# Kernel tuning notes

Hardware: AMD Instinct MI355X
Metric: run time of the kernel (lower is better)

The kernel has to match this reference:

```python
import jax, jax.numpy as jnp
import numpy as np
from jax import lax

B, T, E, H, FD, V = 64, 30, 300, 512, 512, 10000


def setup_inputs() -> dict:
    key = jax.random.key(0)
    ks = iter(jax.random.split(key, 64))

    def nrm(shape, s=0.02):
        return jax.random.normal(next(ks), shape, jnp.float32) * s

    inp = {}
    inp["captions"] = jax.random.randint(next(ks), (B, T), 0, V)
    inp["features"] = jax.random.normal(next(ks), (B, E), jnp.float32)
    inp["h0"] = jax.random.uniform(next(ks), (B, H), jnp.float32)
    inp["c0"] = jax.random.uniform(next(ks), (B, H), jnp.float32)
    inp["B_emb"] = nrm((V, E), 1.0)  # nn.Embedding default N(0,1)
    for g in "ifoc":
        inp[f"V_{g}_W"] = nrm((E, FD)); inp[f"V_{g}_b"] = jnp.zeros((FD,), jnp.float32)
        inp[f"S_{g}_W"] = nrm((FD, FD)); inp[f"S_{g}_b"] = jnp.zeros((FD,), jnp.float32)
        inp[f"U_{g}_W"] = nrm((FD, H)); inp[f"U_{g}_b"] = jnp.zeros((H,), jnp.float32)
        inp[f"W_{g}_W"] = nrm((H, H)); inp[f"W_{g}_b"] = jnp.zeros((H,), jnp.float32)
    inp["C_W"] = nrm((H, V)); inp["C_b"] = jnp.zeros((V,), jnp.float32)
    return inp


def _factored_lstm(captions, features, h0, c0, B_emb,
                   V_i_W, V_i_b, S_i_W, S_i_b, U_i_W, U_i_b, W_i_W, W_i_b,
                   V_f_W, V_f_b, S_f_W, S_f_b, U_f_W, U_f_b, W_f_W, W_f_b,
                   V_o_W, V_o_b, S_o_W, S_o_b, U_o_W, U_o_b, W_o_W, W_o_b,
                   V_c_W, V_c_b, S_c_W, S_c_b, U_c_W, U_c_b, W_c_W, W_c_b,
                   C_W, C_b):
    # mode == 'factual': prepend image features as first timestep
    emb = B_emb[captions]                                       # [B,T,E]
    x = jnp.concatenate([features[:, None, :], emb], axis=1)[:, :-1]  # [B,T,E]

    # input-dependent gate pre-activations: U_g(S_fg(V_g(x))) are h-independent,
    # so precompute them for all timesteps (same math, batched GEMMs).
    def pre(Vw, Vb, Sw, Sb, Uw, Ub):
        f = (x @ Vw + Vb) @ Sw + Sb                             # [B,T,FD]
        return (f @ Uw + Ub).transpose(1, 0, 2)                 # [T,B,H]

    ui = pre(V_i_W, V_i_b, S_i_W, S_i_b, U_i_W, U_i_b)
    uf = pre(V_f_W, V_f_b, S_f_W, S_f_b, U_f_W, U_f_b)
    uo = pre(V_o_W, V_o_b, S_o_W, S_o_b, U_o_W, U_o_b)
    uc = pre(V_c_W, V_c_b, S_c_W, S_c_b, U_c_W, U_c_b)

    def step(carry, u):
        h, c = carry
        gi, gf, go, gc = u
        i_t = jax.nn.sigmoid(gi + h @ W_i_W + W_i_b)
        f_t = jax.nn.sigmoid(gf + h @ W_f_W + W_f_b)
        o_t = jax.nn.sigmoid(go + h @ W_o_W + W_o_b)
        c_tilda = jnp.tanh(gc + h @ W_c_W + W_c_b)
        c_t = f_t * c + i_t * c_tilda
        h_t = o_t * c_t                                         # note: no tanh, as in source
        out = h_t @ C_W + C_b                                   # [B,V]
        return (h_t, c_t), out

    (_, _), outs = lax.scan(step, (h0, c0), (ui, uf, uo, uc))   # outs [T,B,V]
    return outs.transpose(1, 0, 2)                              # [B,T,V]


def reference(captions, features, h0, c0, B_emb,
              V_i_W, V_i_b, S_i_W, S_i_b, U_i_W, U_i_b, W_i_W, W_i_b,
              V_f_W, V_f_b, S_f_W, S_f_b, U_f_W, U_f_b, W_f_W, W_f_b,
              V_o_W, V_o_b, S_o_W, S_o_b, U_o_W, U_o_b, W_o_W, W_o_b,
              V_c_W, V_c_b, S_c_W, S_c_b, U_c_W, U_c_b, W_c_W, W_c_b,
              C_W, C_b):
    return _factored_lstm(captions, features, h0, c0, B_emb,
                          V_i_W, V_i_b, S_i_W, S_i_b, U_i_W, U_i_b, W_i_W, W_i_b,
                          V_f_W, V_f_b, S_f_W, S_f_b, U_f_W, U_f_b, W_f_W, W_f_b,
                          V_o_W, V_o_b, S_o_W, S_o_b, U_o_W, U_o_b, W_o_W, W_o_b,
                          V_c_W, V_c_b, S_c_W, S_c_b, U_c_W, U_c_b, W_c_W, W_c_b,
                          C_W, C_b)
```

## Files before the change

### kernel.cpp

```cpp
#include <hip/hip_runtime.h>
#include <hip/hip_bf16.h>

#define B_  64
#define T_  30
#define E_  300
#define H_  512
#define FD_ 512
#define V_  10000
#define NR_ 32
#define NPW_ 224
#define NTN_ 79
#define NTG_ 8
#define AGGF_ 1056

typedef __attribute__((ext_vector_type(8))) unsigned short ushort8_t;
typedef __attribute__((ext_vector_type(4))) unsigned short ushort4_t;
typedef __attribute__((ext_vector_type(8))) __bf16 bf16x8;
typedef __attribute__((ext_vector_type(4))) float f32x4;

__device__ __forceinline__ float b2f(unsigned short u) {
    union { unsigned int i; float f; } v;
    v.i = ((unsigned int)u) << 16;
    return v.f;
}
__device__ __forceinline__ unsigned short f2b(float f) {
    unsigned int x = __builtin_bit_cast(unsigned int, f);
    unsigned int r = x + 0x7FFFu + ((x >> 16) & 1u);
    return (unsigned short)(r >> 16);
}
__device__ __forceinline__ f32x4 mfma16(bf16x8 a, bf16x8 b, f32x4 c) {
    return __builtin_amdgcn_mfma_f32_16x16x32_bf16(a, b, c, 0, 0, 0);
}

struct PrepA {
    const float* tsrc[17];
    unsigned short* tdst[17];
    const int* captions;
    const float* features;
    const float* Bemb;
    unsigned short* X;
    const float* h0;
    unsigned short* cH0;
    int* bar;
};

__global__ __launch_bounds__(256) void prep_k(PrepA p) {
    const int blk = blockIdx.x, tid = threadIdx.x;
    __shared__ unsigned short tile[32][33];
    if (blk < 8720) {
        int z, bx, by, R, C, Rpad, ld;
        if (blk < 3072) { z = blk >> 8; int wq = blk & 255; bx = wq & 15; by = wq >> 4; R = 512; C = 512; Rpad = 512; ld = 512; }
        else if (blk < 3712) { int b2 = blk - 3072; z = 12 + b2 / 160; int wq = b2 % 160; bx = wq & 15; by = wq >> 4; R = 300; C = 512; Rpad = 320; ld = 320; }
        else { int b2 = blk - 3712; z = 16; bx = b2 % 313; by = b2 / 313; R = 512; C = 10000; Rpad = 512; ld = 512; }
        const float* __restrict__ src = p.tsrc[z];
        unsigned short* __restrict__ dst = p.tdst[z];
        const int tc = tid & 31, tr = tid >> 5;
        const int c0 = bx * 32, r0 = by * 32;
#pragma unroll
        for (int i = 0; i < 4; ++i) {
            int r = r0 + tr + i * 8, c = c0 + tc;
            unsigned short v = 0;
            if (r < R && c < C) v = f2b(src[(size_t)r * C + c]);
            tile[tr + i * 8][tc] = v;
        }
        __syncthreads();
#pragma unroll
        for (int i = 0; i < 4; ++i) {
            int c = c0 + tr + i * 8;
            int r = r0 + tc;
            if (c < C && r < Rpad) dst[(size_t)c * ld + r] = tile[tc][tr + i * 8];
        }
    } else if (blk < 11000) {
        int idx = (blk - 8720) * 256 + tid;
        if (idx < B_ * T_ * 304) {
            int r = idx / 304, e = idx - r * 304;
            int t = r >> 6, b = r & 63;
            float v = 0.f;
            if (e < E_) {
                if (t == 0) v = p.features[b * E_ + e];
                else {
                    int tok = p.captions[b * T_ + (t - 1)];
                    v = p.Bemb[(size_t)tok * E_ + e];
                }
            }
            p.X[(size_t)r * 304 + e] = f2b(v);
        }
    } else {
        int i = (blk - 11000) * 256 + tid;
        if (i < 2048) p.bar[i] = 0;
        if (i < B_ * H_) p.cH0[i] = f2b(p.h0[i]);
    }
}

struct ChainA {
    const unsigned short* X;
    const unsigned short* Vt[4];
    const float* Vb[4];
    const unsigned short* St[4];
    const float* Sb[4];
    const unsigned short* Ut[4];
    const float* Ub[4];
    unsigned short* U[4];
};

__global__ __launch_bounds__(256) void chain_k(ChainA ca) {
    const int rb = blockIdx.x >> 2, g = blockIdx.x & 3;
    __shared__ char pool[66560];
    unsigned short* XT = (unsigned short*)pool;
    unsigned short* R0 = (unsigned short*)pool;
    unsigned short* R1 = (unsigned short*)(pool + 33280);
    const int tid = threadIdx.x;
    const int wv = tid >> 6, lane = tid & 63;
    const int quad = lane >> 4, l16 = lane & 15;

    {
        const unsigned short* src = ca.X + (size_t)rb * 32 * 304;
#pragma unroll
        for (int it = 0; it < 5; ++it) {
            int id = it * 256 + tid;
            int row = id / 40, c8 = (id % 40) * 8;
            ushort8_t v = {0, 0, 0, 0, 0, 0, 0, 0};
            if (c8 < 304) v = *(const ushort8_t*)(src + row * 304 + c8);
            *(ushort8_t*)&XT[row * 328 + c8] = v;
        }
    }
    __syncthreads();
#pragma unroll
    for (int half = 0; half < 2; ++half) {
        const int cb = wv * 128 + half * 64;
        f32x4 acc[2][4] = {};
        for (int kc = 0; kc < 10; ++kc) {
            bf16x8 af[2];
#pragma unroll
            for (int mt = 0; mt < 2; ++mt)
                af[mt] = *(const bf16x8*)&XT[(mt * 16 + l16) * 328 + kc * 32 + quad * 8];
#pragma unroll
            for (int nt = 0; nt < 4; ++nt) {
                bf16x8 bf = *(const bf16x8*)(ca.Vt[g] + (size_t)(cb + nt * 16 + l16) * 320 + kc * 32 + quad * 8);
#pragma unroll
                for (int mt = 0; mt < 2; ++mt) acc[mt][nt] = mfma16(af[mt], bf, acc[mt][nt]);
            }
        }
#pragma unroll
        for (int mt = 0; mt < 2; ++mt)
#pragma unroll
            for (int nt = 0; nt < 4; ++nt) {
                int col = cb + nt * 16 + l16;
                float bv = ca.Vb[g][col];
#pragma unroll
                for (int r = 0; r < 4; ++r)
                    R1[(mt * 16 + quad * 4 + r) * 520 + col] = f2b(acc[mt][nt][r] + bv);
            }
    }
    __syncthreads();
#pragma unroll
    for (int half = 0; half < 2; ++half) {
        const int cb = wv * 128 + half * 64;
        f32x4 acc[2][4] = {};
        for (int kc = 0; kc < 16; ++kc) {
            bf16x8 af[2];
#pragma unroll
            for (int mt = 0; mt < 2; ++mt)
                af[mt] = *(const bf16x8*)&R1[(mt * 16 + l16) * 520 + kc * 32 + quad * 8];
#pragma unroll
            for (int nt = 0; nt < 4; ++nt) {
                bf16x8 bf = *(const bf16x8*)(ca.St[g] + (size_t)(cb + nt * 16 + l16) * 512 + kc * 32 + quad * 8);
#pragma unroll
                for (int mt = 0; mt < 2; ++mt) acc[mt][nt] = mfma16(af[mt], bf, acc[mt][nt]);
            }
        }
        __syncthreads();
#pragma unroll
        for (int mt = 0; mt < 2; ++mt)
#pragma unroll
            for (int nt = 0; nt < 4; ++nt) {
                int col = cb + nt * 16 + l16;
                float bv = ca.Sb[g][col];
#pragma unroll
                for (int r = 0; r < 4; ++r)
                    R0[(mt * 16 + quad * 4 + r) * 520 + col] = f2b(acc[mt][nt][r] + bv);
            }
    }
    __syncthreads();
#pragma unroll
    for (int half = 0; half < 2; ++half) {
        const int cb = wv * 128 + half * 64;
        f32x4 acc[2][4] = {};
        for (int kc = 0; kc < 16; ++kc) {
            bf16x8 af[2];
#pragma unroll
            for (int mt = 0; mt < 2; ++mt)
                af[mt] = *(const bf16x8*)&R0[(mt * 16 + l16) * 520 + kc * 32 + quad * 8];
#pragma unroll
            for (int nt = 0; nt < 4; ++nt) {
                bf16x8 bf = *(const bf16x8*)(ca.Ut[g] + (size_t)(cb + nt * 16 + l16) * 512 + kc * 32 + quad * 8);
#pragma unroll
                for (int mt = 0; mt < 2; ++mt) acc[mt][nt] = mfma16(af[mt], bf, acc[mt][nt]);
            }
        }
#pragma unroll
        for (int mt = 0; mt < 2; ++mt)
#pragma unroll
            for (int nt = 0; nt < 4; ++nt) {
                int col = cb + nt * 16 + l16;
                float bv = ca.Ub[g][col];
#pragma unroll
                for (int r = 0; r < 4; ++r)
                    ca.U[g][(size_t)(rb * 32 + mt * 16 + quad * 4 + r) * 512 + col] =
                        f2b(acc[mt][nt][r] + bv);
            }
    }
}

struct MegaA {
    const unsigned short* h0c;
    const unsigned short* Wt[4];
    const float* Wb[4];
    const unsigned short* U[4];
    const float* c0;
    unsigned short* Hall;
    int* bar;
    const unsigned short* Ct;
    const float* Cb;
    float* out;
};

__global__ __launch_bounds__(256, 1) void mega_k(MegaA a) {
    __shared__ char pool[83712];
    const int tid = threadIdx.x;
    const int lane = tid & 63;
    const int quad = lane >> 4, l16 = lane & 15;

    if (blockIdx.x < NR_) {
        unsigned short* hs = (unsigned short*)pool;
        float* xch = (float*)(pool + 66560);
        const int j = blockIdx.x;
        const int g = tid >> 6;
        bf16x8 afrag[16];
        {
            const unsigned short* wt = a.Wt[g] + (size_t)(j * 16 + l16) * H_ + quad * 8;
#pragma unroll
            for (int kc = 0; kc < 16; ++kc) afrag[kc] = *(const bf16x8*)(wt + kc * 32);
        }
        const int eb = tid >> 2;
        const int ehc = (tid & 3) * 4;
        const int hcg = j * 16 + ehc;
        f32x4 wb[4];
#pragma unroll
        for (int q = 0; q < 4; ++q) wb[q] = *(const f32x4*)(a.Wb[q] + hcg);
        f32x4 c = *(const f32x4*)(a.c0 + (size_t)eb * H_ + hcg);

        for (int t = 0; t < T_; ++t) {
            ushort4_t u[4];
#pragma unroll
            for (int q = 0; q < 4; ++q)
                u[q] = *(const ushort4_t*)(a.U[q] + ((size_t)t * B_ + eb) * H_ + hcg);
            const unsigned short* hp = t ? (a.Hall + (size_t)(t - 1) * B_ * H_) : a.h0c;
#pragma unroll
            for (int it = 0; it < 16; ++it) {
                int id = it * 256 + tid;
                int row = id >> 6, c8 = (id & 63) * 8;
                ushort8_t v = *(const ushort8_t*)(hp + row * H_ + c8);
                *(ushort8_t*)&hs[row * 520 + c8] = v;
            }
            __syncthreads();
            f32x4 acc[4] = {{0.f,0.f,0.f,0.f},{0.f,0.f,0.f,0.f},{0.f,0.f,0.f,0.f},{0.f,0.f,0.f,0.f}};
#pragma unroll
            for (int kc = 0; kc < 16; ++kc) {
#pragma unroll
                for (int nt = 0; nt < 4; ++nt) {
                    bf16x8 bfr = *(const bf16x8*)&hs[(nt * 16 + l16) * 520 + kc * 32 + quad * 8];
                    acc[nt] = mfma16(afrag[kc], bfr, acc[nt]);
                }
            }
#pragma unroll
            for (int nt = 0; nt < 4; ++nt)
#pragma unroll
                for (int r = 0; r < 4; ++r)
                    xch[g * 1040 + (quad * 4 + r) * 65 + nt * 16 + l16] = acc[nt][r];
            __syncthreads();
            ushort4_t hnew;
#pragma unroll
            for (int r = 0; r < 4; ++r) {
                float pi = xch[0 * 1040 + (ehc + r) * 65 + eb] + b2f(u[0][r]) + wb[0][r];
                float pf = xch[1 * 1040 + (ehc + r) * 65 + eb] + b2f(u[1][r]) + wb[1][r];
                float po = xch[2 * 1040 + (ehc + r) * 65 + eb] + b2f(u[2][r]) + wb[2][r];
                float pc = xch[3 * 1040 + (ehc + r) * 65 + eb] + b2f(u[3][r]) + wb[3][r];
                float it = 1.f / (1.f + __expf(-pi));
                float ft = 1.f / (1.f + __expf(-pf));
                float ot = 1.f / (1.f + __expf(-po));
                float ct = tanhf(pc);
                float cn = ft * c[r] + it * ct;
                c[r] = cn;
                hnew[r] = f2b(ot * cn);
            }
            {
                union { ushort4_t s4; unsigned long long q; } hu;
                hu.s4 = hnew;
                __hip_atomic_store((unsigned long long*)(a.Hall + ((size_t)t * B_ + eb) * H_ + hcg),
                                   hu.q, __ATOMIC_RELAXED, __HIP_MEMORY_SCOPE_AGENT);
            }
            asm volatile("s_waitcnt vmcnt(0)" ::: "memory");
            __syncthreads();
            if (tid == 0)
                __hip_atomic_store(&a.bar[j], t + 1, __ATOMIC_RELAXED, __HIP_MEMORY_SCOPE_AGENT);
            if (t + 1 < T_ || j == 0) {
                if (g == 0) {
                    bool done;
                    do {
                        int v = __hip_atomic_load(&a.bar[lane & 31], __ATOMIC_RELAXED, __HIP_MEMORY_SCOPE_AGENT);
                        done = __all(v >= t + 1);
                        if (!done) __builtin_amdgcn_s_sleep(1);
                    } while (!done);
                    if (j == 0 && lane == 0)
                        __hip_atomic_store(&a.bar[AGGF_], t + 1, __ATOMIC_RELAXED, __HIP_MEMORY_SCOPE_AGENT);
                }
                if (t + 1 < T_) __syncthreads();
            }
        }
    } else {
        unsigned short* As = (unsigned short*)pool;
        unsigned short* Bs = (unsigned short*)(pool + 36864);
        const int wv = tid >> 6;
        const int mw = (wv & 1) * 32, nw = (wv >> 1) * 64;
        const int NJ = NTG_ * NTN_;
        int hiF = 0;
        for (int q = (int)blockIdx.x - NR_; q < NJ; q += NPW_) {
            const int tg = q / NTN_, n0 = (q % NTN_) * 128;
            const int tb = tg * 4;
            const int need = (tb + 4 < T_) ? tb + 4 : T_;
            if (need > hiF) {
                if (tid < 64) {
                    while (__hip_atomic_load(&a.bar[AGGF_], __ATOMIC_RELAXED, __HIP_MEMORY_SCOPE_AGENT) < need)
                        __builtin_amdgcn_s_sleep(8);
                }
                __syncthreads();
                hiF = need;
            }
            f32x4 acc[4][2][4] = {};
            for (int k0 = 0; k0 < H_; k0 += 64) {
#pragma unroll
                for (int tt = 0; tt < 4; ++tt) {
                    int tA = tb + tt; if (tA >= T_) tA = T_ - 1;
                    const unsigned short* Ap = a.Hall + (size_t)tA * B_ * H_;
                    int id = tid;
#pragma unroll
                    for (int it = 0; it < 2; ++it, id += 256) {
                        int row = id >> 3, c8 = (id & 7) * 8;
                        *(ushort8_t*)&As[tt * 4608 + row * 72 + c8] =
                            *(const ushort8_t*)(Ap + (size_t)row * H_ + k0 + c8);
                    }
                }
                {
                    int id2 = tid;
#pragma unroll
                    for (int it = 0; it < 4; ++it, id2 += 256) {
                        int row = id2 >> 3, c8 = (id2 & 7) * 8;
                        int gn = n0 + row;
                        ushort8_t v = {0, 0, 0, 0, 0, 0, 0, 0};
                        if (gn < V_) v = *(const ushort8_t*)(a.Ct + (size_t)gn * H_ + k0 + c8);
                        *(ushort8_t*)&Bs[row * 72 + c8] = v;
                    }
                }
                __syncthreads();
#pragma unroll
                for (int kk = 0; kk < 2; ++kk) {
                    bf16x8 bf[4];
#pragma unroll
                    for (int nt = 0; nt < 4; ++nt)
                        bf[nt] = *(const bf16x8*)&Bs[(nw + nt * 16 + l16) * 72 + kk * 32 + quad * 8];
#pragma unroll
                    for (int tt = 0; tt < 4; ++tt) {
                        bf16x8 af[2];
#pragma unroll
                        for (int mt = 0; mt < 2; ++mt)
                            af[mt] = *(const bf16x8*)&As[tt * 4608 + (mw + mt * 16 + l16) * 72 + kk * 32 + quad * 8];
#pragma unroll
                        for (int mt = 0; mt < 2; ++mt)
#pragma unroll
                            for (int nt = 0; nt < 4; ++nt)
                                acc[tt][mt][nt] = mfma16(af[mt], bf[nt], acc[tt][mt][nt]);
                    }
                }
                __syncthreads();
            }
#pragma unroll
            for (int tt = 0; tt < 4; ++tt) {
                const int t = tb + tt;
                if (t >= T_) continue;
#pragma unroll
                for (int mt = 0; mt < 2; ++mt)
#pragma unroll
                    for (int nt = 0; nt < 4; ++nt) {
                        int col = n0 + nw + nt * 16 + l16;
                        if (col >= V_) continue;
                        float bv = a.Cb[col];
                        int bb = mw + mt * 16 + quad * 4;
#pragma unroll
                        for (int r = 0; r < 4; ++r) {
                            int orow = (bb + r) * T_ + t;
                            a.out[(size_t)orow * V_ + col] = acc[tt][mt][nt][r] + bv;
                        }
                    }
            }
        }
    }
}

extern "C" void kernel_launch(void* const* d_in, const int* in_sizes, int n_in,
                              void* d_out, int out_size, void* d_ws, size_t ws_size,
                              hipStream_t stream) {
    (void)in_sizes; (void)n_in; (void)out_size; (void)ws_size;
    const int* captions = (const int*)d_in[0];
    const float* features = (const float*)d_in[1];
    const float* h0 = (const float*)d_in[2];
    const float* c0 = (const float*)d_in[3];
    const float* Bemb = (const float*)d_in[4];
    const float *iVW[4], *iVb[4], *iSW[4], *iSb[4], *iUW[4], *iUb[4], *iWW[4], *iWb[4];
    for (int g = 0; g < 4; ++g) {
        const int base = 5 + 8 * g;
        iVW[g] = (const float*)d_in[base + 0];
        iVb[g] = (const float*)d_in[base + 1];
        iSW[g] = (const float*)d_in[base + 2];
        iSb[g] = (const float*)d_in[base + 3];
        iUW[g] = (const float*)d_in[base + 4];
        iUb[g] = (const float*)d_in[base + 5];
        iWW[g] = (const float*)d_in[base + 6];
        iWb[g] = (const float*)d_in[base + 7];
    }
    const float* CW = (const float*)d_in[37];
    const float* Cb = (const float*)d_in[38];

    char* w = (char*)d_ws;
    auto alloc = [&](size_t bytes) -> void* {
        void* p = (void*)w;
        w += (bytes + 255) & ~(size_t)255;
        return p;
    };
    int* dbar = (int*)alloc(8192);
    unsigned short* cH0 = (unsigned short*)alloc((size_t)B_ * H_ * 2);
    unsigned short *wVt[4], *wSt[4], *wUt[4], *wWt[4];
    for (int g = 0; g < 4; ++g) wVt[g] = (unsigned short*)alloc((size_t)FD_ * 320 * 2);
    for (int g = 0; g < 4; ++g) wSt[g] = (unsigned short*)alloc((size_t)FD_ * FD_ * 2);
    for (int g = 0; g < 4; ++g) wUt[g] = (unsigned short*)alloc((size_t)H_ * FD_ * 2);
    for (int g = 0; g < 4; ++g) wWt[g] = (unsigned short*)alloc((size_t)H_ * H_ * 2);
    unsigned short* wCt = (unsigned short*)alloc((size_t)V_ * H_ * 2);
    unsigned short* wX = (unsigned short*)alloc((size_t)B_ * T_ * 304 * 2);
    unsigned short* bufA[4];
    for (int g = 0; g < 4; ++g) bufA[g] = (unsigned short*)alloc((size_t)B_ * T_ * FD_ * 2);
    unsigned short* Hall = (unsigned short*)alloc((size_t)B_ * T_ * H_ * 2);

    {
        PrepA p{};
        for (int g = 0; g < 4; ++g) {
            p.tsrc[g * 3 + 0] = iSW[g]; p.tdst[g * 3 + 0] = wSt[g];
            p.tsrc[g * 3 + 1] = iUW[g]; p.tdst[g * 3 + 1] = wUt[g];
            p.tsrc[g * 3 + 2] = iWW[g]; p.tdst[g * 3 + 2] = wWt[g];
            p.tsrc[12 + g] = iVW[g];    p.tdst[12 + g] = wVt[g];
        }
        p.tsrc[16] = CW; p.tdst[16] = wCt;
        p.captions = captions; p.features = features; p.Bemb = Bemb; p.X = wX;
        p.h0 = h0; p.cH0 = cH0; p.bar = dbar;
        prep_k<<<dim3(11128), 256, 0, stream>>>(p);
    }

    {
        ChainA ca{};
        ca.X = wX;
        for (int g = 0; g < 4; ++g) {
            ca.Vt[g] = wVt[g]; ca.Vb[g] = iVb[g];
            ca.St[g] = wSt[g]; ca.Sb[g] = iSb[g];
            ca.Ut[g] = wUt[g]; ca.Ub[g] = iUb[g];
            ca.U[g] = bufA[g];
        }
        chain_k<<<dim3(240), 256, 0, stream>>>(ca);
    }

    {
        MegaA ma{};
        ma.h0c = cH0;
        for (int g = 0; g < 4; ++g) {
            ma.Wt[g] = wWt[g]; ma.Wb[g] = iWb[g]; ma.U[g] = bufA[g];
        }
        ma.c0 = c0;
        ma.Hall = Hall;
        ma.bar = dbar;
        ma.Ct = wCt;
        ma.Cb = Cb;
        ma.out = (float*)d_out;
        mega_k<<<dim3(NR_ + NPW_), 256, 0, stream>>>(ma);
    }
}
```

Before: 413.9 us.

## Split fused recurrence/projection megakernel into separate recurrence and projection kernels

Replaces the persistent megakernel, in which 224 worker blocks spin-waited on the recurrence's progress flags to overlap the vocabulary projection with the LSTM steps, with two launches. A 32-block recurrence kernel runs all timesteps, then a standard 128x128-tile GEMM kernel computes the full [T*B, V] projection with 1185 blocks. This drops the polling and the 4-timestep grouping in exchange for losing the overlap of the projection with the serial recurrence. It adds a kernel launch boundary.

```diff
diff --git a/kernel.cpp b/kernel.cpp
--- a/kernel.cpp
+++ b/kernel.cpp
@@ -8,10 +8,8 @@
 #define FD_ 512
 #define V_  10000
 #define NR_ 32
-#define NPW_ 224
 #define NTN_ 79
-#define NTG_ 8
-#define AGGF_ 1056
+#define NTM_ 15
 
 typedef __attribute__((ext_vector_type(8))) unsigned short ushort8_t;
 typedef __attribute__((ext_vector_type(4))) unsigned short ushort4_t;
@@ -212,7 +210,7 @@
     }
 }
 
-struct MegaA {
+struct RecA {
     const unsigned short* h0c;
     const unsigned short* Wt[4];
     const float* Wb[4];
@@ -220,191 +218,167 @@
     const float* c0;
     unsigned short* Hall;
     int* bar;
+};
+
+__global__ __launch_bounds__(256, 1) void rec_k(RecA a) {
+    __shared__ char pool[83712];
+    const int tid = threadIdx.x;
+    const int lane = tid & 63;
+    const int quad = lane >> 4, l16 = lane & 15;
+    unsigned short* hs = (unsigned short*)pool;
+    float* xch = (float*)(pool + 66560);
+    const int j = blockIdx.x;
+    const int g = tid >> 6;
+    bf16x8 afrag[16];
+    {
+        const unsigned short* wt = a.Wt[g] + (size_t)(j * 16 + l16) * H_ + quad * 8;
+#pragma unroll
+        for (int kc = 0; kc < 16; ++kc) afrag[kc] = *(const bf16x8*)(wt + kc * 32);
+    }
+    const int eb = tid >> 2;
+    const int ehc = (tid & 3) * 4;
+    const int hcg = j * 16 + ehc;
+    f32x4 wb[4];
+#pragma unroll
+    for (int q = 0; q < 4; ++q) wb[q] = *(const f32x4*)(a.Wb[q] + hcg);
+    f32x4 c = *(const f32x4*)(a.c0 + (size_t)eb * H_ + hcg);
+
+    for (int t = 0; t < T_; ++t) {
+        ushort4_t u[4];
+#pragma unroll
+        for (int q = 0; q < 4; ++q)
+            u[q] = *(const ushort4_t*)(a.U[q] + ((size_t)t * B_ + eb) * H_ + hcg);
+        const unsigned short* hp = t ? (a.Hall + (size_t)(t - 1) * B_ * H_) : a.h0c;
+#pragma unroll
+        for (int it = 0; it < 16; ++it) {
+            int id = it * 256 + tid;
+            int row = id >> 6, c8 = (id & 63) * 8;
+            ushort8_t v = *(const ushort8_t*)(hp + row * H_ + c8);
+            *(ushort8_t*)&hs[row * 520 + c8] = v;
+        }
+        __syncthreads();
+        f32x4 acc[4] = {{0.f,0.f,0.f,0.f},{0.f,0.f,0.f,0.f},{0.f,0.f,0.f,0.f},{0.f,0.f,0.f,0.f}};
+#pragma unroll
+        for (int kc = 0; kc < 16; ++kc) {
+#pragma unroll
+            for (int nt = 0; nt < 4; ++nt) {
+                bf16x8 bfr = *(const bf16x8*)&hs[(nt * 16 + l16) * 520 + kc * 32 + quad * 8];
+                acc[nt] = mfma16(afrag[kc], bfr, acc[nt]);
+            }
+        }
+#pragma unroll
+        for (int nt = 0; nt < 4; ++nt)
+#pragma unroll
+            for (int r = 0; r < 4; ++r)
+                xch[g * 1040 + (quad * 4 + r) * 65 + nt * 16 + l16] = acc[nt][r];
+        __syncthreads();
+        ushort4_t hnew;
+#pragma unroll
+        for (int r = 0; r < 4; ++r) {
+            float pi = xch[0 * 1040 + (ehc + r) * 65 + eb] + b2f(u[0][r]) + wb[0][r];
+            float pf = xch[1 * 1040 + (ehc + r) * 65 + eb] + b2f(u[1][r]) + wb[1][r];
+            float po = xch[2 * 1040 + (ehc + r) * 65 + eb] + b2f(u[2][r]) + wb[2][r];
+            float pc = xch[3 * 1040 + (ehc + r) * 65 + eb] + b2f(u[3][r]) + wb[3][r];
+            float it = 1.f / (1.f + __expf(-pi));
+            float ft = 1.f / (1.f + __expf(-pf));
+            float ot = 1.f / (1.f + __expf(-po));
+            float ct = tanhf(pc);
+            float cn = ft * c[r] + it * ct;
+            c[r] = cn;
+            hnew[r] = f2b(ot * cn);
+        }
+        {
+            union { ushort4_t s4; unsigned long long q; } hu;
+            hu.s4 = hnew;
+            __hip_atomic_store((unsigned long long*)(a.Hall + ((size_t)t * B_ + eb) * H_ + hcg),
+                               hu.q, __ATOMIC_RELAXED, __HIP_MEMORY_SCOPE_AGENT);
+        }
+        asm volatile("s_waitcnt vmcnt(0)" ::: "memory");
+        __syncthreads();
+        if (t + 1 < T_) {
+            if (tid == 0)
+                __hip_atomic_store(&a.bar[j], t + 1, __ATOMIC_RELAXED, __HIP_MEMORY_SCOPE_AGENT);
+            if (g == 0) {
+                bool done;
+                do {
+                    int v = __hip_atomic_load(&a.bar[lane & 31], __ATOMIC_RELAXED, __HIP_MEMORY_SCOPE_AGENT);
+                    done = __all(v >= t + 1);
+                    if (!done) __builtin_amdgcn_s_sleep(1);
+                } while (!done);
+            }
+            __syncthreads();
+        }
+    }
+}
+
+struct ProjA {
+    const unsigned short* Hall;
     const unsigned short* Ct;
     const float* Cb;
     float* out;
 };
 
-__global__ __launch_bounds__(256, 1) void mega_k(MegaA a) {
-    __shared__ char pool[83712];
+__global__ __launch_bounds__(256) void proj_k(ProjA a) {
+    __shared__ unsigned short As[128 * 72];
+    __shared__ unsigned short Bs[128 * 72];
     const int tid = threadIdx.x;
-    const int lane = tid & 63;
+    const int lane = tid & 63, wv = tid >> 6;
     const int quad = lane >> 4, l16 = lane & 15;
-
-    if (blockIdx.x < NR_) {
-        unsigned short* hs = (unsigned short*)pool;
-        float* xch = (float*)(pool + 66560);
-        const int j = blockIdx.x;
-        const int g = tid >> 6;
-        bf16x8 afrag[16];
+    const int mq = (wv & 1) * 64, nq = (wv >> 1) * 64;
+    const int m0 = ((int)blockIdx.x / NTN_) * 128;
+    const int n0 = ((int)blockIdx.x % NTN_) * 128;
+    f32x4 acc[4][4] = {};
+    for (int k0 = 0; k0 < H_; k0 += 64) {
         {
-            const unsigned short* wt = a.Wt[g] + (size_t)(j * 16 + l16) * H_ + quad * 8;
-#pragma unroll
-            for (int kc = 0; kc < 16; ++kc) afrag[kc] = *(const bf16x8*)(wt + kc * 32);
-        }
-        const int eb = tid >> 2;
-        const int ehc = (tid & 3) * 4;
-        const int hcg = j * 16 + ehc;
-        f32x4 wb[4];
-#pragma unroll
-        for (int q = 0; q < 4; ++q) wb[q] = *(const f32x4*)(a.Wb[q] + hcg);
-        f32x4 c = *(const f32x4*)(a.c0 + (size_t)eb * H_ + hcg);
-
-        for (int t = 0; t < T_; ++t) {
-            ushort4_t u[4];
-#pragma unroll
-            for (int q = 0; q < 4; ++q)
-                u[q] = *(const ushort4_t*)(a.U[q] + ((size_t)t * B_ + eb) * H_ + hcg);
-            const unsigned short* hp = t ? (a.Hall + (size_t)(t - 1) * B_ * H_) : a.h0c;
-#pragma unroll
-            for (int it = 0; it < 16; ++it) {
-                int id = it * 256 + tid;
-                int row = id >> 6, c8 = (id & 63) * 8;
-                ushort8_t v = *(const ushort8_t*)(hp + row * H_ + c8);
-                *(ushort8_t*)&hs[row * 520 + c8] = v;
-            }
-            __syncthreads();
-            f32x4 acc[4] = {{0.f,0.f,0.f,0.f},{0.f,0.f,0.f,0.f},{0.f,0.f,0.f,0.f},{0.f,0.f,0.f,0.f}};
-#pragma unroll
-            for (int kc = 0; kc < 16; ++kc) {
-#pragma unroll
-                for (int nt = 0; nt < 4; ++nt) {
-                    bf16x8 bfr = *(const bf16x8*)&hs[(nt * 16 + l16) * 520 + kc * 32 + quad * 8];
-                    acc[nt] = mfma16(afrag[kc], bfr, acc[nt]);
-                }
-            }
+            int id = tid;
+#pragma unroll
+            for (int it = 0; it < 4; ++it, id += 256) {
+                int row = id >> 3, c8 = (id & 7) * 8;
+                *(ushort8_t*)&As[row * 72 + c8] =
+                    *(const ushort8_t*)(a.Hall + (size_t)(m0 + row) * H_ + k0 + c8);
+            }
+            int id2 = tid;
+#pragma unroll
+            for (int it = 0; it < 4; ++it, id2 += 256) {
+                int row = id2 >> 3, c8 = (id2 & 7) * 8;
+                int gn = n0 + row;
+                ushort8_t v = {0, 0, 0, 0, 0, 0, 0, 0};
+                if (gn < V_) v = *(const ushort8_t*)(a.Ct + (size_t)gn * H_ + k0 + c8);
+                *(ushort8_t*)&Bs[row * 72 + c8] = v;
+            }
+        }
+        __syncthreads();
+#pragma unroll
+        for (int kk = 0; kk < 2; ++kk) {
+            bf16x8 af[4], bf[4];
+#pragma unroll
+            for (int mt = 0; mt < 4; ++mt)
+                af[mt] = *(const bf16x8*)&As[(mq + mt * 16 + l16) * 72 + kk * 32 + quad * 8];
 #pragma unroll
             for (int nt = 0; nt < 4; ++nt)
-#pragma unroll
-                for (int r = 0; r < 4; ++r)
-                    xch[g * 1040 + (quad * 4 + r) * 65 + nt * 16 + l16] = acc[nt][r];
-            __syncthreads();
-            ushort4_t hnew;
+                bf[nt] = *(const bf16x8*)&Bs[(nq + nt * 16 + l16) * 72 + kk * 32 + quad * 8];
+#pragma unroll
+            for (int mt = 0; mt < 4; ++mt)
+#pragma unroll
+                for (int nt = 0; nt < 4; ++nt)
+                    acc[mt][nt] = mfma16(af[mt], bf[nt], acc[mt][nt]);
+        }
+        __syncthreads();
+    }
+#pragma unroll
+    for (int mt = 0; mt < 4; ++mt)
+#pragma unroll
+        for (int nt = 0; nt < 4; ++nt) {
+            int col = n0 + nq + nt * 16 + l16;
+            if (col >= V_) continue;
+            float bv = a.Cb[col];
 #pragma unroll
             for (int r = 0; r < 4; ++r) {
-                float pi = xch[0 * 1040 + (ehc + r) * 65 + eb] + b2f(u[0][r]) + wb[0][r];
-                float pf = xch[1 * 1040 + (ehc + r) * 65 + eb] + b2f(u[1][r]) + wb[1][r];
-                float po = xch[2 * 1040 + (ehc + r) * 65 + eb] + b2f(u[2][r]) + wb[2][r];
-                float pc = xch[3 * 1040 + (ehc + r) * 65 + eb] + b2f(u[3][r]) + wb[3][r];
-                float it = 1.f / (1.f + __expf(-pi));
-                float ft = 1.f / (1.f + __expf(-pf));
-                float ot = 1.f / (1.f + __expf(-po));
-                float ct = tanhf(pc);
-                float cn = ft * c[r] + it * ct;
-                c[r] = cn;
-                hnew[r] = f2b(ot * cn);
-            }
-            {
-                union { ushort4_t s4; unsigned long long q; } hu;
-                hu.s4 = hnew;
-                __hip_atomic_store((unsigned long long*)(a.Hall + ((size_t)t * B_ + eb) * H_ + hcg),
-                                   hu.q, __ATOMIC_RELAXED, __HIP_MEMORY_SCOPE_AGENT);
-            }
-            asm volatile("s_waitcnt vmcnt(0)" ::: "memory");
-            __syncthreads();
-            if (tid == 0)
-                __hip_atomic_store(&a.bar[j], t + 1, __ATOMIC_RELAXED, __HIP_MEMORY_SCOPE_AGENT);
-            if (t + 1 < T_ || j == 0) {
-                if (g == 0) {
-                    bool done;
-                    do {
-                        int v = __hip_atomic_load(&a.bar[lane & 31], __ATOMIC_RELAXED, __HIP_MEMORY_SCOPE_AGENT);
-                        done = __all(v >= t + 1);
-                        if (!done) __builtin_amdgcn_s_sleep(1);
-                    } while (!done);
-                    if (j == 0 && lane == 0)
-                        __hip_atomic_store(&a.bar[AGGF_], t + 1, __ATOMIC_RELAXED, __HIP_MEMORY_SCOPE_AGENT);
-                }
-                if (t + 1 < T_) __syncthreads();
-            }
-        }
-    } else {
-        unsigned short* As = (unsigned short*)pool;
-        unsigned short* Bs = (unsigned short*)(pool + 36864);
-        const int wv = tid >> 6;
-        const int mw = (wv & 1) * 32, nw = (wv >> 1) * 64;
-        const int NJ = NTG_ * NTN_;
-        int hiF = 0;
-        for (int q = (int)blockIdx.x - NR_; q < NJ; q += NPW_) {
-            const int tg = q / NTN_, n0 = (q % NTN_) * 128;
-            const int tb = tg * 4;
-            const int need = (tb + 4 < T_) ? tb + 4 : T_;
-            if (need > hiF) {
-                if (tid < 64) {
-                    while (__hip_atomic_load(&a.bar[AGGF_], __ATOMIC_RELAXED, __HIP_MEMORY_SCOPE_AGENT) < need)
-                        __builtin_amdgcn_s_sleep(8);
-                }
-                __syncthreads();
-                hiF = need;
-            }
-            f32x4 acc[4][2][4] = {};
-            for (int k0 = 0; k0 < H_; k0 += 64) {
-#pragma unroll
-                for (int tt = 0; tt < 4; ++tt) {
-                    int tA = tb + tt; if (tA >= T_) tA = T_ - 1;
-                    const unsigned short* Ap = a.Hall + (size_t)tA * B_ * H_;
-                    int id = tid;
-#pragma unroll
-                    for (int it = 0; it < 2; ++it, id += 256) {
-                        int row = id >> 3, c8 = (id & 7) * 8;
-                        *(ushort8_t*)&As[tt * 4608 + row * 72 + c8] =
-                            *(const ushort8_t*)(Ap + (size_t)row * H_ + k0 + c8);
-                    }
-                }
-                {
-                    int id2 = tid;
-#pragma unroll
-                    for (int it = 0; it < 4; ++it, id2 += 256) {
-                        int row = id2 >> 3, c8 = (id2 & 7) * 8;
-                        int gn = n0 + row;
-                        ushort8_t v = {0, 0, 0, 0, 0, 0, 0, 0};
-                        if (gn < V_) v = *(const ushort8_t*)(a.Ct + (size_t)gn * H_ + k0 + c8);
-                        *(ushort8_t*)&Bs[row * 72 + c8] = v;
-                    }
-                }
-                __syncthreads();
-#pragma unroll
-                for (int kk = 0; kk < 2; ++kk) {
-                    bf16x8 bf[4];
-#pragma unroll
-                    for (int nt = 0; nt < 4; ++nt)
-                        bf[nt] = *(const bf16x8*)&Bs[(nw + nt * 16 + l16) * 72 + kk * 32 + quad * 8];
-#pragma unroll
-                    for (int tt = 0; tt < 4; ++tt) {
-                        bf16x8 af[2];
-#pragma unroll
-                        for (int mt = 0; mt < 2; ++mt)
-                            af[mt] = *(const bf16x8*)&As[tt * 4608 + (mw + mt * 16 + l16) * 72 + kk * 32 + quad * 8];
-#pragma unroll
-                        for (int mt = 0; mt < 2; ++mt)
-#pragma unroll
-                            for (int nt = 0; nt < 4; ++nt)
-                                acc[tt][mt][nt] = mfma16(af[mt], bf[nt], acc[tt][mt][nt]);
-                    }
-                }
-                __syncthreads();
-            }
-#pragma unroll
-            for (int tt = 0; tt < 4; ++tt) {
-                const int t = tb + tt;
-                if (t >= T_) continue;
-#pragma unroll
-                for (int mt = 0; mt < 2; ++mt)
-#pragma unroll
-                    for (int nt = 0; nt < 4; ++nt) {
-                        int col = n0 + nw + nt * 16 + l16;
-                        if (col >= V_) continue;
-                        float bv = a.Cb[col];
-                        int bb = mw + mt * 16 + quad * 4;
-#pragma unroll
-                        for (int r = 0; r < 4; ++r) {
-                            int orow = (bb + r) * T_ + t;
-                            a.out[(size_t)orow * V_ + col] = acc[tt][mt][nt][r] + bv;
-                        }
-                    }
-            }
-        }
-    }
+                int m = m0 + mq + mt * 16 + quad * 4 + r;
+                int t = m >> 6, b = m & 63;
+                a.out[(size_t)(b * T_ + t) * V_ + col] = acc[mt][nt][r] + bv;
+            }
+        }
 }
 
 extern "C" void kernel_launch(void* const* d_in, const int* in_sizes, int n_in,
@@ -477,17 +451,23 @@
     }
 
     {
-        MegaA ma{};
-        ma.h0c = cH0;
+        RecA ra{};
+        ra.h0c = cH0;
         for (int g = 0; g < 4; ++g) {
-            ma.Wt[g] = wWt[g]; ma.Wb[g] = iWb[g]; ma.U[g] = bufA[g];
-        }
-        ma.c0 = c0;
-        ma.Hall = Hall;
-        ma.bar = dbar;
-        ma.Ct = wCt;
-        ma.Cb = Cb;
-        ma.out = (float*)d_out;
-        mega_k<<<dim3(NR_ + NPW_), 256, 0, stream>>>(ma);
-    }
-}
+            ra.Wt[g] = wWt[g]; ra.Wb[g] = iWb[g]; ra.U[g] = bufA[g];
+        }
+        ra.c0 = c0;
+        ra.Hall = Hall;
+        ra.bar = dbar;
+        rec_k<<<dim3(NR_), 256, 0, stream>>>(ra);
+    }
+
+    {
+        ProjA pa{};
+        pa.Hall = Hall;
+        pa.Ct = wCt;
+        pa.Cb = Cb;
+        pa.out = (float*)d_out;
+        proj_k<<<dim3(NTM_ * NTN_), 256, 0, stream>>>(pa);
+    }
+}
```

New measurement: 448.7 us. 1.08x slower.

## Overlap C_W transpose with recurrence and fuse embedding gather into chain kernel

Applied to the files above, without the earlier changes.

Moves the fp32-to-bf16 transpose of the large output projection matrix C_W out of the prep kernel and into the idle output-GEMM blocks of the persistent mega kernel. Those blocks do the transpose while the recurrence blocks run, then meet at a global counter barrier before starting the output GEMMs. The embedding gather and bf16 conversion also move from prep into chain_k, which removes the intermediate X buffer and its round trip through global memory. The cost is that all 224 worker blocks must be co-resident for the spin barrier, and chain_k now does scattered fp32 gathers.

```diff
diff --git a/kernel.cpp b/kernel.cpp
--- a/kernel.cpp
+++ b/kernel.cpp
@@ -12,6 +12,8 @@
 #define NTN_ 79
 #define NTG_ 8
 #define AGGF_ 1056
+#define PCNT_ 1088
+#define CWT_  5008
 
 typedef __attribute__((ext_vector_type(8))) unsigned short ushort8_t;
 typedef __attribute__((ext_vector_type(4))) unsigned short ushort4_t;
@@ -33,12 +35,8 @@
 }
 
 struct PrepA {
-    const float* tsrc[17];
-    unsigned short* tdst[17];
-    const int* captions;
-    const float* features;
-    const float* Bemb;
-    unsigned short* X;
+    const float* tsrc[16];
+    unsigned short* tdst[16];
     const float* h0;
     unsigned short* cH0;
     int* bar;
@@ -47,11 +45,10 @@
 __global__ __launch_bounds__(256) void prep_k(PrepA p) {
     const int blk = blockIdx.x, tid = threadIdx.x;
     __shared__ unsigned short tile[32][33];
-    if (blk < 8720) {
+    if (blk < 3712) {
         int z, bx, by, R, C, Rpad, ld;
         if (blk < 3072) { z = blk >> 8; int wq = blk & 255; bx = wq & 15; by = wq >> 4; R = 512; C = 512; Rpad = 512; ld = 512; }
-        else if (blk < 3712) { int b2 = blk - 3072; z = 12 + b2 / 160; int wq = b2 % 160; bx = wq & 15; by = wq >> 4; R = 300; C = 512; Rpad = 320; ld = 320; }
-        else { int b2 = blk - 3712; z = 16; bx = b2 % 313; by = b2 / 313; R = 512; C = 10000; Rpad = 512; ld = 512; }
+        else { int b2 = blk - 3072; z = 12 + b2 / 160; int wq = b2 % 160; bx = wq & 15; by = wq >> 4; R = 300; C = 512; Rpad = 320; ld = 320; }
         const float* __restrict__ src = p.tsrc[z];
         unsigned short* __restrict__ dst = p.tdst[z];
         const int tc = tid & 31, tr = tid >> 5;
@@ -70,30 +67,17 @@
             int r = r0 + tc;
             if (c < C && r < Rpad) dst[(size_t)c * ld + r] = tile[tc][tr + i * 8];
         }
-    } else if (blk < 11000) {
-        int idx = (blk - 8720) * 256 + tid;
-        if (idx < B_ * T_ * 304) {
-            int r = idx / 304, e = idx - r * 304;
-            int t = r >> 6, b = r & 63;
-            float v = 0.f;
-            if (e < E_) {
-                if (t == 0) v = p.features[b * E_ + e];
-                else {
-                    int tok = p.captions[b * T_ + (t - 1)];
-                    v = p.Bemb[(size_t)tok * E_ + e];
-                }
-            }
-            p.X[(size_t)r * 304 + e] = f2b(v);
-        }
     } else {
-        int i = (blk - 11000) * 256 + tid;
+        int i = (blk - 3712) * 256 + tid;
         if (i < 2048) p.bar[i] = 0;
         if (i < B_ * H_) p.cH0[i] = f2b(p.h0[i]);
     }
 }
 
 struct ChainA {
-    const unsigned short* X;
+    const int* captions;
+    const float* features;
+    const float* Bemb;
     const unsigned short* Vt[4];
     const float* Vb[4];
     const unsigned short* St[4];
@@ -114,13 +98,34 @@
     const int quad = lane >> 4, l16 = lane & 15;
 
     {
-        const unsigned short* src = ca.X + (size_t)rb * 32 * 304;
+        const int rows0 = rb * 32;
 #pragma unroll
         for (int it = 0; it < 5; ++it) {
             int id = it * 256 + tid;
             int row = id / 40, c8 = (id % 40) * 8;
+            int gr = rows0 + row;
+            int t = gr >> 6, b = gr & 63;
             ushort8_t v = {0, 0, 0, 0, 0, 0, 0, 0};
-            if (c8 < 304) v = *(const ushort8_t*)(src + row * 304 + c8);
+            if (c8 < 304) {
+                const float* src;
+                if (t == 0) src = ca.features + (size_t)b * E_;
+                else {
+                    int tok = ca.captions[b * T_ + (t - 1)];
+                    src = ca.Bemb + (size_t)tok * E_;
+                }
+                if (c8 + 8 <= E_) {
+                    f32x4 aa = *(const f32x4*)(src + c8);
+                    f32x4 bb = *(const f32x4*)(src + c8 + 4);
+                    v[0] = f2b(aa[0]); v[1] = f2b(aa[1]); v[2] = f2b(aa[2]); v[3] = f2b(aa[3]);
+                    v[4] = f2b(bb[0]); v[5] = f2b(bb[1]); v[6] = f2b(bb[2]); v[7] = f2b(bb[3]);
+                } else {
+#pragma unroll
+                    for (int i2 = 0; i2 < 8; ++i2) {
+                        int e = c8 + i2;
+                        if (e < E_) v[i2] = f2b(src[e]);
+                    }
+                }
+            }
             *(ushort8_t*)&XT[row * 328 + c8] = v;
         }
     }
@@ -220,7 +225,8 @@
     const float* c0;
     unsigned short* Hall;
     int* bar;
-    const unsigned short* Ct;
+    const float* CW;
+    unsigned short* Ct;
     const float* Cb;
     float* out;
 };
@@ -319,13 +325,51 @@
             }
         }
     } else {
+        const int w = (int)blockIdx.x - NR_;
+        {
+            unsigned short (*tile)[33] = (unsigned short(*)[33])pool;
+            for (int tb2 = w; tb2 < CWT_; tb2 += NPW_) {
+                const int bx = tb2 % 313, by = tb2 / 313;
+                const int c0 = bx * 32, r0 = by * 32;
+                const int tc = tid & 31, tr = tid >> 5;
+                __syncthreads();
+#pragma unroll
+                for (int i = 0; i < 4; ++i) {
+                    int r = r0 + tr + i * 8, c = c0 + tc;
+                    unsigned short v = 0;
+                    if (c < V_) v = f2b(a.CW[(size_t)r * V_ + c]);
+                    tile[tr + i * 8][tc] = v;
+                }
+                __syncthreads();
+                {
+                    int cl = tid >> 3, rch = (tid & 7) * 4;
+                    int c = c0 + cl;
+                    if (c < V_) {
+                        union { unsigned short s[4]; unsigned long long q; } pk;
+#pragma unroll
+                        for (int k = 0; k < 4; ++k) pk.s[k] = tile[rch + k][cl];
+                        __hip_atomic_store((unsigned long long*)(a.Ct + (size_t)c * H_ + r0 + rch),
+                                           pk.q, __ATOMIC_RELAXED, __HIP_MEMORY_SCOPE_AGENT);
+                    }
+                }
+            }
+            asm volatile("s_waitcnt vmcnt(0)" ::: "memory");
+            __syncthreads();
+            if (tid == 0)
+                __hip_atomic_fetch_add(&a.bar[PCNT_], 1, __ATOMIC_RELAXED, __HIP_MEMORY_SCOPE_AGENT);
+            if (tid < 64) {
+                while (__hip_atomic_load(&a.bar[PCNT_], __ATOMIC_RELAXED, __HIP_MEMORY_SCOPE_AGENT) < NPW_)
+                    __builtin_amdgcn_s_sleep(4);
+            }
+            __syncthreads();
+        }
         unsigned short* As = (unsigned short*)pool;
         unsigned short* Bs = (unsigned short*)(pool + 36864);
         const int wv = tid >> 6;
         const int mw = (wv & 1) * 32, nw = (wv >> 1) * 64;
         const int NJ = NTG_ * NTN_;
         int hiF = 0;
-        for (int q = (int)blockIdx.x - NR_; q < NJ; q += NPW_) {
+        for (int q = w; q < NJ; q += NPW_) {
             const int tg = q / NTN_, n0 = (q % NTN_) * 128;
             const int tb = tg * 4;
             const int need = (tb + 4 < T_) ? tb + 4 : T_;
@@ -445,7 +489,6 @@
     for (int g = 0; g < 4; ++g) wUt[g] = (unsigned short*)alloc((size_t)H_ * FD_ * 2);
     for (int g = 0; g < 4; ++g) wWt[g] = (unsigned short*)alloc((size_t)H_ * H_ * 2);
     unsigned short* wCt = (unsigned short*)alloc((size_t)V_ * H_ * 2);
-    unsigned short* wX = (unsigned short*)alloc((size_t)B_ * T_ * 304 * 2);
     unsigned short* bufA[4];
     for (int g = 0; g < 4; ++g) bufA[g] = (unsigned short*)alloc((size_t)B_ * T_ * FD_ * 2);
     unsigned short* Hall = (unsigned short*)alloc((size_t)B_ * T_ * H_ * 2);
@@ -458,15 +501,13 @@
             p.tsrc[g * 3 + 2] = iWW[g]; p.tdst[g * 3 + 2] = wWt[g];
             p.tsrc[12 + g] = iVW[g];    p.tdst[12 + g] = wVt[g];
         }
-        p.tsrc[16] = CW; p.tdst[16] = wCt;
-        p.captions = captions; p.features = features; p.Bemb = Bemb; p.X = wX;
         p.h0 = h0; p.cH0 = cH0; p.bar = dbar;
-        prep_k<<<dim3(11128), 256, 0, stream>>>(p);
+        prep_k<<<dim3(3840), 256, 0, stream>>>(p);
     }
 
     {
         ChainA ca{};
-        ca.X = wX;
+        ca.captions = captions; ca.features = features; ca.Bemb = Bemb;
         for (int g = 0; g < 4; ++g) {
             ca.Vt[g] = wVt[g]; ca.Vb[g] = iVb[g];
             ca.St[g] = wSt[g]; ca.Sb[g] = iSb[g];
@@ -485,6 +526,7 @@
         ma.c0 = c0;
         ma.Hall = Hall;
         ma.bar = dbar;
+        ma.CW = CW;
         ma.Ct = wCt;
         ma.Cb = Cb;
         ma.out = (float*)d_out;
```

Result: slower. 434.5 us (+5.0%).
